# Performance work log

Hardware: AMD Instinct MI355X
Metric: run time of the kernel (lower is better)

## Reference

```python
import jax, jax.numpy as jnp
import numpy as np

SE, SD, B = 400, 50, 32
H, IN, A = 512, 512, 128
VF, V = 1024, 32000

def _p(k, shape):
    return jax.random.normal(k, shape, dtype=jnp.float32) * 0.02

def setup_inputs() -> dict:
    key = jax.random.key(0)
    ks = jax.random.split(key, 24)
    inp = {
        'output_enc': jax.random.normal(ks[0], (SE, B, 2 * H), dtype=jnp.float32),
        'input_dec': jax.random.normal(ks[1], (SD, B, IN), dtype=jnp.float32),
        'hidden_enc': jax.random.normal(ks[2], (4, B, H), dtype=jnp.float32),
        'cell_state_enc': jax.random.normal(ks[3], (4, B, H), dtype=jnp.float32),
        # LSTM layer 0 (PyTorch gate order i,f,g,o)
        'W_ih0': _p(ks[4], (4 * H, IN)), 'W_hh0': _p(ks[5], (4 * H, H)),
        'b_ih0': _p(ks[6], (4 * H,)), 'b_hh0': _p(ks[7], (4 * H,)),
        # LSTM layer 1
        'W_ih1': _p(ks[8], (4 * H, H)), 'W_hh1': _p(ks[9], (4 * H, H)),
        'b_ih1': _p(ks[10], (4 * H,)), 'b_hh1': _p(ks[11], (4 * H,)),
        # reduce_dim: 2H -> H
        'W_red': _p(ks[12], (H, 2 * H)), 'b_red': _p(ks[13], (H,)),
        # attention: 3H -> A, attn_out: A -> 1 (no bias)
        'W_att': _p(ks[14], (A, 3 * H)), 'b_att': _p(ks[15], (A,)),
        'v_att': _p(ks[16], (1, A)),
        # vocab MLP: 3H -> VF -> V
        'W_v1': _p(ks[17], (VF, 3 * H)), 'b_v1': _p(ks[18], (VF,)),
        'W_v2': _p(ks[19], (V, VF)), 'b_v2': _p(ks[20], (V,)),
    }
    return inp

def _forward(output_enc, input_dec, hidden_enc, cell_state_enc,
             W_ih0, W_hh0, b_ih0, b_hh0, W_ih1, W_hh1, b_ih1, b_hh1,
             W_red, b_red, W_att, b_att, v_att, W_v1, b_v1, W_v2, b_v2):
    # first_word=True path: fold bidirectional encoder state [4,B,H] -> [2,B,2H] -> [2,B,H]
    old_enc = jnp.concatenate([hidden_enc[0:2], hidden_enc[2:]], axis=-1)
    old_cell = jnp.concatenate([cell_state_enc[0:2], cell_state_enc[2:]], axis=-1)
    new_enc = old_enc @ W_red.T + b_red    # [2,B,H]
    new_cell = old_cell @ W_red.T + b_red  # [2,B,H]

    def lstm_cell(x, h, c, W_ih, W_hh, b_ih, b_hh):
        g = x @ W_ih.T + h @ W_hh.T + b_ih + b_hh
        i, f, gg, o = jnp.split(g, 4, axis=-1)
        c_new = jax.nn.sigmoid(f) * c + jax.nn.sigmoid(i) * jnp.tanh(gg)
        h_new = jax.nn.sigmoid(o) * jnp.tanh(c_new)
        return h_new, c_new

    def step(carry, x_t):
        h0, c0, h1, c1 = carry
        h0, c0 = lstm_cell(x_t, h0, c0, W_ih0, W_hh0, b_ih0, b_hh0)
        h1, c1 = lstm_cell(h0, h1, c1, W_ih1, W_hh1, b_ih1, b_hh1)
        return (h0, c0, h1, c1), h1

    init = (new_enc[0], new_cell[0], new_enc[1], new_cell[1])
    (h0f, c0f, h1f, c1f), output_dec = jax.lax.scan(step, init, input_dec)
    hidden_dec = jnp.stack([h0f, h1f])       # [2,B,H]
    cell_state_dec = jnp.stack([c0f, c1f])   # [2,B,H]

    # Additive (Bahdanau) attention, batched over all decoder timesteps.
    # cat order is (output_enc, output_dec) -> first 2H cols of W_att hit encoder.
    enc_part = output_enc @ W_att[:, :2 * H].T              # [Se,B,A]
    dec_part = output_dec @ W_att[:, 2 * H:].T + b_att       # [Sd,B,A]
    e = jnp.tanh(enc_part[:, None] + dec_part[None])         # [Se,Sd,B,A]
    e = jnp.einsum('stba,a->stb', e, v_att[0])               # [Se,Sd,B]
    attn = jax.nn.softmax(e, axis=0)                         # softmax over encoder dim
    context = jnp.einsum('stb,sbe->tbe', attn, output_enc)   # [Sd,B,2H]

    pv_in = jnp.concatenate([output_dec, context], axis=-1)  # [Sd,B,3H]
    pvocab = (pv_in @ W_v1.T + b_v1) @ W_v2.T + b_v2         # [Sd,B,V]
    return pvocab, (hidden_dec, cell_state_dec)

def reference(output_enc, input_dec, hidden_enc, cell_state_enc,
              W_ih0, W_hh0, b_ih0, b_hh0, W_ih1, W_hh1, b_ih1, b_hh1,
              W_red, b_red, W_att, b_att, v_att, W_v1, b_v1, W_v2, b_v2):
    return _forward(output_enc, input_dec, hidden_enc, cell_state_enc,
                    W_ih0, W_hh0, b_ih0, b_hh0, W_ih1, W_hh1, b_ih1, b_hh1,
                    W_red, b_red, W_att, b_att, v_att, W_v1, b_v1, W_v2, b_v2)
```

## Files before the change

### kernel.cpp

```cpp
#include <hip/hip_runtime.h>
#include <cstdint>

#define DEV __device__ __forceinline__

typedef short bfrag __attribute__((ext_vector_type(8)));
typedef float ffrag __attribute__((ext_vector_type(4)));

constexpr int SE = 400, SD = 50, BB = 32;
constexpr int HH = 512, INW = 512, AA = 128;
constexpr int VF = 1024, VV = 32000;
constexpr int G4 = 2048;

DEV ushort f2bf(float f) {
    uint32_t u = __float_as_uint(f);
    u = (u + 0x7FFF + ((u >> 16) & 1)) >> 16;
    return (ushort)u;
}
DEV float bf2f(ushort u) { return __uint_as_float(((uint32_t)u) << 16); }
DEV float sigm_(float x) { return 1.f / (1.f + __expf(-x)); }
DEV float tanh_(float x) { float e = __expf(2.f * x); return 1.f - 2.f / (e + 1.f); }
DEV int imin(int a, int b) { return a < b ? a : b; }
DEV int imax(int a, int b) { return a > b ? a : b; }

DEV void gload_lds16(const void* g, void* l) {
    __builtin_amdgcn_global_load_lds((const __attribute__((address_space(1))) uint32_t*)g,
                                     (__attribute__((address_space(3))) uint32_t*)l, 16, 0, 0);
}

__global__ __launch_bounds__(256) void k_cvt_flat(const float* __restrict__ s,
                                                  ushort* __restrict__ d, long n4) {
    long i = (long)blockIdx.x * 256 + threadIdx.x;
    if (i >= n4) return;
    float4 v = ((const float4*)s)[i];
    ushort4 o;
    o.x = f2bf(v.x); o.y = f2bf(v.y); o.z = f2bf(v.z); o.w = f2bf(v.w);
    ((ushort4*)d)[i] = o;
}

__global__ __launch_bounds__(256) void k_cvt_strided(const float* __restrict__ s,
                                                     ushort* __restrict__ d,
                                                     int rows, int cols, int sstride, int soff,
                                                     int dstride, int doff) {
    int i = blockIdx.x * 256 + threadIdx.x;
    int c4n = cols >> 2;
    if (i >= rows * c4n) return;
    int r = i / c4n, c = (i - r * c4n) * 4;
    float4 v = *(const float4*)(s + (size_t)r * sstride + soff + c);
    ushort4 o;
    o.x = f2bf(v.x); o.y = f2bf(v.y); o.z = f2bf(v.z); o.w = f2bf(v.w);
    *(ushort4*)(d + (size_t)r * dstride + doff + c) = o;
}

__global__ __launch_bounds__(256) void k_bsum(const float* __restrict__ bi0, const float* __restrict__ bh0,
                                              const float* __restrict__ bi1, const float* __restrict__ bh1,
                                              float* __restrict__ bsum0, float* __restrict__ bsum1) {
    int i = blockIdx.x * 256 + threadIdx.x;
    if (i >= G4) return;
    bsum0[i] = bi0[i] + bh0[i];
    bsum1[i] = bi1[i] + bh1[i];
}

__global__ __launch_bounds__(256) void k_fold(const float* __restrict__ hid,
                                              const float* __restrict__ cel,
                                              const float* __restrict__ W_red,
                                              const float* __restrict__ b_red,
                                              float* __restrict__ h0m,
                                              float* __restrict__ c0, float* __restrict__ c1,
                                              ushort* __restrict__ AB) {
    int tid = threadIdx.x;
    int j = blockIdx.x * 256 + tid;
    int b = blockIdx.y;
    int l = blockIdx.z & 1;
    bool is_c = blockIdx.z >> 1;
    const float* src = is_c ? cel : hid;
    __shared__ float xs[1024];
    for (int i = tid; i < 512; i += 256) {
        xs[i]       = src[((size_t)l * BB + b) * HH + i];
        xs[512 + i] = src[((size_t)(l + 2) * BB + b) * HH + i];
    }
    __syncthreads();
    const float4* w  = (const float4*)(W_red + (size_t)j * 1024);
    const float4* xv = (const float4*)xs;
    float acc = b_red[j];
    for (int k = 0; k < 256; k++) {
        float4 a = w[k], x = xv[k];
        acc += a.x * x.x + a.y * x.y + a.z * x.z + a.w * x.w;
    }
    if (is_c) {
        (l ? c1 : c0)[(size_t)b * HH + j] = acc;
    } else {
        if (l == 0) {
            h0m[(size_t)b * HH + j] = acc;
            AB[(size_t)32 * 1024 + (size_t)b * 1024 + j] = f2bf(acc);
        } else {
            AB[(size_t)b * 1024 + 512 + j] = f2bf(acc);
        }
    }
}

__global__ __launch_bounds__(256) void k_cell(const ushort* __restrict__ Aprev,
                                              const ushort* __restrict__ W0,
                                              const ushort* __restrict__ W1,
                                              const float* __restrict__ gx,
                                              const float* __restrict__ bsum1,
                                              float* __restrict__ c0, float* __restrict__ c1,
                                              float* __restrict__ h0m,
                                              float* __restrict__ od1,
                                              ushort* __restrict__ od1_bf,
                                              ushort* __restrict__ ABdst,
                                              int do_l0, int do_l1) {
    const int layer = blockIdx.y;
    if (layer == 0 && !do_l0) return;
    if (layer == 1 && !do_l1) return;
    const int jb = blockIdx.x;
    const int tid = threadIdx.x, wave = tid >> 6, lane = tid & 63;
    const int lr = lane & 15, lk = lane >> 4;
    const int K = layer ? 1024 : 512;
    const ushort* Wm = layer ? W1 : W0;
    const int wstride = layer ? 1024 : 512;
    const int n0 = wave * 512 + jb * 16;

    const ushort* arow0 = Aprev + (size_t)lr * 1024;
    const ushort* arow1 = Aprev + (size_t)(16 + lr) * 1024;
    const ushort* wrow  = Wm + (size_t)(n0 + lr) * wstride;

    ffrag acc0 = {0.f, 0.f, 0.f, 0.f}, acc1 = {0.f, 0.f, 0.f, 0.f};
    #pragma unroll 4
    for (int k0 = 0; k0 < K; k0 += 32) {
        bfrag a0 = *(const bfrag*)(arow0 + k0 + lk * 8);
        bfrag a1 = *(const bfrag*)(arow1 + k0 + lk * 8);
        bfrag bw = *(const bfrag*)(wrow + k0 + lk * 8);
        acc0 = __builtin_amdgcn_mfma_f32_16x16x32_bf16(a0, bw, acc0, 0, 0, 0);
        acc1 = __builtin_amdgcn_mfma_f32_16x16x32_bf16(a1, bw, acc1, 0, 0, 0);
    }

    __shared__ float gl[4][32][16];
    #pragma unroll
    for (int r = 0; r < 4; r++) {
        gl[wave][lk * 4 + r][lr]      = acc0[r];
        gl[wave][16 + lk * 4 + r][lr] = acc1[r];
    }
    __syncthreads();

    for (int e = tid; e < 512; e += 256) {
        int b = e >> 4, jj = e & 15;
        int j = jb * 16 + jj;
        float gi = gl[0][b][jj], gf = gl[1][b][jj], gg = gl[2][b][jj], go = gl[3][b][jj];
        if (layer == 0) {
            const float* gxp = gx + (size_t)b * G4;
            gi += gxp[j]; gf += gxp[512 + j]; gg += gxp[1024 + j]; go += gxp[1536 + j];
        } else {
            gi += bsum1[j]; gf += bsum1[512 + j]; gg += bsum1[1024 + j]; go += bsum1[1536 + j];
        }
        float* cc = layer ? c1 : c0;
        size_t ci = (size_t)b * HH + j;
        float cn = sigm_(gf) * cc[ci] + sigm_(gi) * tanh_(gg);
        cc[ci] = cn;
        float hn = sigm_(go) * tanh_(cn);
        ushort hb = f2bf(hn);
        if (layer == 0) {
            h0m[ci] = hn;
            ABdst[(size_t)b * 1024 + j] = hb;
        } else {
            od1[ci] = hn;
            od1_bf[ci] = hb;
            ABdst[(size_t)b * 1024 + 512 + j] = hb;
        }
    }
}

__global__ __launch_bounds__(256) void k_states(const float* __restrict__ h0,
                                                const float* __restrict__ h1,
                                                const float* __restrict__ c0,
                                                const float* __restrict__ c1,
                                                float* __restrict__ out) {
    int i = blockIdx.x * 256 + threadIdx.x;
    if (i >= BB * HH) return;
    out[i]               = h0[i];
    out[BB * HH + i]     = h1[i];
    out[2 * BB * HH + i] = c0[i];
    out[3 * BB * HH + i] = c1[i];
}

template <int OUT_BF16>
__global__ __launch_bounds__(256) void k_gemm128(const ushort* __restrict__ X,
                                                 const ushort* __restrict__ W,
                                                 float* __restrict__ Cf,
                                                 ushort* __restrict__ Cb,
                                                 const float* __restrict__ bias,
                                                 int M, int N, int K, int nmt) {
    __shared__ ushort As[128 * 32];
    __shared__ ushort Bs[128 * 32];
    const int tid = threadIdx.x;
    const int wave = tid >> 6, lane = tid & 63;
    const int lr = lane & 15, lk = lane >> 4;
    const int wm = wave >> 1, wn = wave & 1;

    int nwg = gridDim.x, flat = blockIdx.x;
    int q = nwg >> 3, r = nwg & 7;
    int xcd = flat & 7, idx = flat >> 3;
    int wg = (xcd < r ? xcd * (q + 1) : r * (q + 1) + (xcd - r) * q) + idx;
    const int m0 = (wg % nmt) * 128, n0 = (wg / nmt) * 128;

    ffrag acc[4][4];
    #pragma unroll
    for (int i = 0; i < 4; i++)
        #pragma unroll
        for (int j = 0; j < 4; j++) acc[i][j] = (ffrag){0.f, 0.f, 0.f, 0.f};

    const int srow = wave * 16 + (lane >> 2);
    const int scol = (lane & 3) * 8;
    const int ar0 = imin(m0 + srow, M - 1);
    const int ar1 = imin(m0 + 64 + srow, M - 1);
    const ushort* Agp0 = X + (size_t)ar0 * K + scol;
    const ushort* Agp1 = X + (size_t)ar1 * K + scol;
    const ushort* Bgp0 = W + (size_t)(n0 + srow) * K + scol;
    const ushort* Bgp1 = W + (size_t)(n0 + 64 + srow) * K + scol;
    ushort* AsW0 = As + wave * 512;
    ushort* AsW1 = As + 2048 + wave * 512;
    ushort* BsW0 = Bs + wave * 512;
    ushort* BsW1 = Bs + 2048 + wave * 512;

    for (int k0 = 0; k0 < K; k0 += 32) {
        gload_lds16(Agp0 + k0, AsW0);
        gload_lds16(Agp1 + k0, AsW1);
        gload_lds16(Bgp0 + k0, BsW0);
        gload_lds16(Bgp1 + k0, BsW1);
        __syncthreads();
        bfrag a[4], bfr[4];
        #pragma unroll
        for (int mf = 0; mf < 4; mf++)
            a[mf] = *(const bfrag*)&As[(wm * 64 + mf * 16 + lr) * 32 + lk * 8];
        #pragma unroll
        for (int nf = 0; nf < 4; nf++)
            bfr[nf] = *(const bfrag*)&Bs[(wn * 64 + nf * 16 + lr) * 32 + lk * 8];
        #pragma unroll
        for (int mf = 0; mf < 4; mf++)
            #pragma unroll
            for (int nf = 0; nf < 4; nf++)
                acc[mf][nf] = __builtin_amdgcn_mfma_f32_16x16x32_bf16(a[mf], bfr[nf], acc[mf][nf], 0, 0, 0);
        __syncthreads();
    }

    #pragma unroll
    for (int mf = 0; mf < 4; mf++) {
        int rbase = m0 + wm * 64 + mf * 16 + lk * 4;
        #pragma unroll
        for (int nf = 0; nf < 4; nf++) {
            int cc = n0 + wn * 64 + nf * 16 + lr;
            float bv = bias ? bias[cc] : 0.f;
            #pragma unroll
            for (int rr = 0; rr < 4; rr++) {
                int row = rbase + rr;
                if (row < M) {
                    float v = acc[mf][nf][rr] + bv;
                    if (OUT_BF16) Cb[(size_t)row * N + cc] = f2bf(v);
                    else          Cf[(size_t)row * N + cc] = v;
                }
            }
        }
    }
}

__global__ __launch_bounds__(256) void k_scores(const float* __restrict__ encp,
                                                const float* __restrict__ decp,
                                                const float* __restrict__ v_att,
                                                float* __restrict__ attn) {
    int t = blockIdx.x, b = blockIdx.y, tid = threadIdx.x;
    __shared__ float dp[128], vv[128];
    __shared__ float e_lds[400];
    __shared__ float red[8];
    if (tid < 128) {
        dp[tid] = decp[((size_t)t * BB + b) * AA + tid];
        vv[tid] = v_att[tid];
    }
    __syncthreads();
    for (int s = tid; s < SE; s += 256) {
        const float* ep = encp + ((size_t)s * BB + b) * AA;
        float a0 = 0.f;
        #pragma unroll 4
        for (int a = 0; a < AA; a++) a0 += vv[a] * tanh_(ep[a] + dp[a]);
        e_lds[s] = a0;
    }
    __syncthreads();
    float m = -1e30f;
    for (int s = tid; s < SE; s += 256) m = fmaxf(m, e_lds[s]);
    #pragma unroll
    for (int o = 32; o > 0; o >>= 1) m = fmaxf(m, __shfl_xor(m, o));
    if ((tid & 63) == 0) red[tid >> 6] = m;
    __syncthreads();
    m = fmaxf(fmaxf(red[0], red[1]), fmaxf(red[2], red[3]));
    float sum = 0.f;
    for (int s = tid; s < SE; s += 256) {
        float ex = __expf(e_lds[s] - m);
        e_lds[s] = ex;
        sum += ex;
    }
    #pragma unroll
    for (int o = 32; o > 0; o >>= 1) sum += __shfl_xor(sum, o);
    if ((tid & 63) == 0) red[4 + (tid >> 6)] = sum;
    __syncthreads();
    float inv = 1.f / (red[4] + red[5] + red[6] + red[7]);
    for (int s = tid; s < SE; s += 256)
        attn[((size_t)b * SD + t) * SE + s] = e_lds[s] * inv;
}

__global__ __launch_bounds__(256) void k_context(const float* __restrict__ attn,
                                                 const ushort* __restrict__ oe_bf,
                                                 float* __restrict__ ctx) {
    int b = blockIdx.x, nc = blockIdx.y, th = blockIdx.z, tid = threadIdx.x;
    __shared__ float at[25][400];
    const float* ap = attn + ((size_t)b * SD + th * 25) * SE;
    for (int i = tid; i < 25 * 400; i += 256) at[i / 400][i % 400] = ap[i];
    __syncthreads();
    int n = nc * 256 + tid;
    float acc[25];
    #pragma unroll
    for (int i = 0; i < 25; i++) acc[i] = 0.f;
    for (int s = 0; s < SE; s++) {
        float v = bf2f(oe_bf[((size_t)s * BB + b) * 1024 + n]);
        #pragma unroll
        for (int tt = 0; tt < 25; tt++) acc[tt] += at[tt][s] * v;
    }
    #pragma unroll
    for (int tt = 0; tt < 25; tt++)
        ctx[(((size_t)(th * 25 + tt)) * BB + b) * 1024 + n] = acc[tt];
}

__global__ __launch_bounds__(256) void k_concat(const ushort* __restrict__ od_bf,
                                                const float* __restrict__ ctx,
                                                ushort* __restrict__ x1) {
    int i = blockIdx.x * 256 + threadIdx.x;
    if (i >= 1600 * 384) return;
    int rr = i / 384, c4 = (i - rr * 384) * 4;
    ushort4 o;
    if (c4 < 512) {
        o = *(const ushort4*)(od_bf + (size_t)rr * 512 + c4);
    } else {
        float4 v = *(const float4*)(ctx + (size_t)rr * 1024 + (c4 - 512));
        o.x = f2bf(v.x); o.y = f2bf(v.y); o.z = f2bf(v.z); o.w = f2bf(v.w);
    }
    *(ushort4*)(x1 + (size_t)rr * 1536 + c4) = o;
}

extern "C" void kernel_launch(void* const* d_in, const int* in_sizes, int n_in,
                              void* d_out, int out_size, void* d_ws, size_t ws_size,
                              hipStream_t stream) {
    const float* output_enc = (const float*)d_in[0];
    const float* input_dec  = (const float*)d_in[1];
    const float* hidden_enc = (const float*)d_in[2];
    const float* cell_enc   = (const float*)d_in[3];
    const float* W_ih0 = (const float*)d_in[4],  *W_hh0 = (const float*)d_in[5];
    const float* b_ih0 = (const float*)d_in[6],  *b_hh0 = (const float*)d_in[7];
    const float* W_ih1 = (const float*)d_in[8],  *W_hh1 = (const float*)d_in[9];
    const float* b_ih1 = (const float*)d_in[10], *b_hh1 = (const float*)d_in[11];
    const float* W_red = (const float*)d_in[12], *b_red = (const float*)d_in[13];
    const float* W_att = (const float*)d_in[14], *b_att = (const float*)d_in[15];
    const float* v_att = (const float*)d_in[16];
    const float* W_v1  = (const float*)d_in[17], *b_v1 = (const float*)d_in[18];
    const float* W_v2  = (const float*)d_in[19], *b_v2 = (const float*)d_in[20];

    char* ws = (char*)d_ws;
    size_t off = 0;
    auto alloc = [&](size_t bytes) -> void* {
        void* p = ws + off;
        off += (bytes + 255) & ~(size_t)255;
        return p;
    };
    float*  h0m    = (float*)alloc(BB * HH * 4);
    float*  c0     = (float*)alloc(BB * HH * 4);
    float*  c1     = (float*)alloc(BB * HH * 4);
    ushort* AB     = (ushort*)alloc(2 * BB * 1024 * 2);
    float*  od     = (float*)alloc((size_t)SD * BB * HH * 4);
    ushort* od_bf  = (ushort*)alloc((size_t)SD * BB * HH * 2);
    ushort* xd_bf  = (ushort*)alloc((size_t)SD * BB * INW * 2);
    ushort* wih0b  = (ushort*)alloc((size_t)G4 * 512 * 2);
    ushort* whh0b  = (ushort*)alloc((size_t)G4 * 512 * 2);
    ushort* w1cat  = (ushort*)alloc((size_t)G4 * 1024 * 2);
    float*  bsum0  = (float*)alloc(G4 * 4);
    float*  bsum1  = (float*)alloc(G4 * 4);
    float*  gx0    = (float*)alloc((size_t)SD * BB * G4 * 4);
    ushort* oe_bf  = (ushort*)alloc((size_t)SE * BB * 1024 * 2);
    ushort* wae    = (ushort*)alloc((size_t)AA * 1024 * 2);
    ushort* wad    = (ushort*)alloc((size_t)AA * 512 * 2);
    float*  encp   = (float*)alloc((size_t)SE * BB * AA * 4);
    float*  decp   = (float*)alloc((size_t)SD * BB * AA * 4);
    float*  attn   = (float*)alloc((size_t)BB * SD * SE * 4);
    float*  ctx    = (float*)alloc((size_t)SD * BB * 1024 * 4);
    ushort* x1     = (ushort*)alloc((size_t)1600 * 1536 * 2);
    ushort* wv1    = (ushort*)alloc((size_t)VF * 1536 * 2);
    ushort* y1     = (ushort*)alloc((size_t)1600 * VF * 2);
    ushort* wv2    = (ushort*)alloc((size_t)VV * 1024 * 2);

    k_cvt_flat<<<800, 256, 0, stream>>>(input_dec, xd_bf, (long)SD * BB * INW / 4);
    k_cvt_flat<<<12800, 256, 0, stream>>>(output_enc, oe_bf, (long)SE * BB * 1024 / 4);
    k_cvt_flat<<<1024, 256, 0, stream>>>(W_ih0, wih0b, (long)G4 * 512 / 4);
    k_cvt_flat<<<1024, 256, 0, stream>>>(W_hh0, whh0b, (long)G4 * 512 / 4);
    k_cvt_strided<<<1024, 256, 0, stream>>>(W_ih1, w1cat, G4, 512, 512, 0, 1024, 0);
    k_cvt_strided<<<1024, 256, 0, stream>>>(W_hh1, w1cat, G4, 512, 512, 0, 1024, 512);
    k_cvt_strided<<<128, 256, 0, stream>>>(W_att, wae, AA, 1024, 1536, 0, 1024, 0);
    k_cvt_strided<<<64, 256, 0, stream>>>(W_att, wad, AA, 512, 1536, 1024, 512, 0);
    k_cvt_flat<<<1536, 256, 0, stream>>>(W_v1, wv1, (long)VF * 1536 / 4);
    k_cvt_flat<<<32000, 256, 0, stream>>>(W_v2, wv2, (long)VV * 1024 / 4);
    k_bsum<<<8, 256, 0, stream>>>(b_ih0, b_hh0, b_ih1, b_hh1, bsum0, bsum1);

    k_fold<<<dim3(2, 32, 4), 256, 0, stream>>>(hidden_enc, cell_enc, W_red, b_red,
                                               h0m, c0, c1, AB);

    k_gemm128<0><<<13 * 16, 256, 0, stream>>>(xd_bf, wih0b, gx0, nullptr, bsum0,
                                              SD * BB, G4, 512, 13);

    for (int i = 0; i <= SD; i++) {
        const ushort* Aprev = AB + (size_t)((i + 1) & 1) * BB * 1024;
        ushort* ABdst = AB + (size_t)(i & 1) * BB * 1024;
        int t1c = (i > 0) ? (i - 1) : 0;
        k_cell<<<dim3(32, 2), 256, 0, stream>>>(Aprev, whh0b, w1cat,
                                                gx0 + (size_t)i * BB * G4, bsum1,
                                                c0, c1, h0m,
                                                od + (size_t)t1c * BB * HH,
                                                od_bf + (size_t)t1c * BB * HH,
                                                ABdst, (int)(i < SD), (int)(i > 0));
    }
    k_states<<<64, 256, 0, stream>>>(h0m, od + (size_t)(SD - 1) * BB * HH, c0, c1,
                                     (float*)d_out + (size_t)SD * BB * VV);

    k_gemm128<0><<<100, 256, 0, stream>>>(oe_bf, wae, encp, nullptr,
                                          (const float*)nullptr, SE * BB, AA, 1024, 100);
    k_gemm128<0><<<13, 256, 0, stream>>>(od_bf, wad, decp, nullptr,
                                         b_att, SD * BB, AA, 512, 13);
    k_scores<<<dim3(SD, BB), 256, 0, stream>>>(encp, decp, v_att, attn);
    k_context<<<dim3(32, 4, 2), 256, 0, stream>>>(attn, oe_bf, ctx);

    k_concat<<<2400, 256, 0, stream>>>(od_bf, ctx, x1);
    k_gemm128<1><<<13 * 8, 256, 0, stream>>>(x1, wv1, nullptr, y1, b_v1,
                                             1600, VF, 1536, 13);
    k_gemm128<0><<<13 * 250, 256, 0, stream>>>(y1, wv2, (float*)d_out, nullptr, b_v2,
                                               1600, VV, 1024, 13);
    (void)in_sizes; (void)n_in; (void)out_size; (void)ws_size;
}
```

Before: 1.669 ms.

## Batch conversions, double-buffer GEMM, fuse concat into producers, vectorize scores

The ten conversion launches are merged into two multi-segment kernels that find their segment from a per-launch table. The bf16 GEMM now double-buffers its LDS tiles, so the next K-tile loads while the current one is computed. The LSTM cell and context kernels write bf16 directly into the concatenated vocab-MLP input, which removes the fp32 context buffer and the separate concat kernel. The scores loop reads float4 vectors and the context loop is unrolled by four. The cost is double the GEMM shared memory, which may lower occupancy.

```diff
diff --git a/kernel.cpp b/kernel.cpp
--- a/kernel.cpp
+++ b/kernel.cpp
@@ -20,35 +20,47 @@
 DEV float sigm_(float x) { return 1.f / (1.f + __expf(-x)); }
 DEV float tanh_(float x) { float e = __expf(2.f * x); return 1.f - 2.f / (e + 1.f); }
 DEV int imin(int a, int b) { return a < b ? a : b; }
-DEV int imax(int a, int b) { return a > b ? a : b; }
 
 DEV void gload_lds16(const void* g, void* l) {
     __builtin_amdgcn_global_load_lds((const __attribute__((address_space(1))) uint32_t*)g,
                                      (__attribute__((address_space(3))) uint32_t*)l, 16, 0, 0);
 }
 
-__global__ __launch_bounds__(256) void k_cvt_flat(const float* __restrict__ s,
-                                                  ushort* __restrict__ d, long n4) {
-    long i = (long)blockIdx.x * 256 + threadIdx.x;
-    if (i >= n4) return;
-    float4 v = ((const float4*)s)[i];
+struct CvtFlatTab {
+    const float* src[6];
+    ushort* dst[6];
+    int blk_end[6];
+    int nseg;
+};
+__global__ __launch_bounds__(256) void k_cvt_multi(CvtFlatTab t) {
+    int blk = blockIdx.x, seg = 0;
+    while (seg < t.nseg - 1 && blk >= t.blk_end[seg]) seg++;
+    int base = seg ? t.blk_end[seg - 1] : 0;
+    long i = (long)(blk - base) * 256 + threadIdx.x;
+    float4 v = ((const float4*)t.src[seg])[i];
     ushort4 o;
     o.x = f2bf(v.x); o.y = f2bf(v.y); o.z = f2bf(v.z); o.w = f2bf(v.w);
-    ((ushort4*)d)[i] = o;
-}
-
-__global__ __launch_bounds__(256) void k_cvt_strided(const float* __restrict__ s,
-                                                     ushort* __restrict__ d,
-                                                     int rows, int cols, int sstride, int soff,
-                                                     int dstride, int doff) {
-    int i = blockIdx.x * 256 + threadIdx.x;
-    int c4n = cols >> 2;
-    if (i >= rows * c4n) return;
+    ((ushort4*)t.dst[seg])[i] = o;
+}
+
+struct CvtStrTab {
+    const float* src[4];
+    ushort* dst[4];
+    int ss[4], so[4], ds[4], dofs[4], c4n[4];
+    int blk_end[4];
+    int nseg;
+};
+__global__ __launch_bounds__(256) void k_cvt_str_multi(CvtStrTab t) {
+    int blk = blockIdx.x, seg = 0;
+    while (seg < t.nseg - 1 && blk >= t.blk_end[seg]) seg++;
+    int base = seg ? t.blk_end[seg - 1] : 0;
+    int i = (blk - base) * 256 + threadIdx.x;
+    int c4n = t.c4n[seg];
     int r = i / c4n, c = (i - r * c4n) * 4;
-    float4 v = *(const float4*)(s + (size_t)r * sstride + soff + c);
+    float4 v = *(const float4*)(t.src[seg] + (size_t)r * t.ss[seg] + t.so[seg] + c);
     ushort4 o;
     o.x = f2bf(v.x); o.y = f2bf(v.y); o.z = f2bf(v.z); o.w = f2bf(v.w);
-    *(ushort4*)(d + (size_t)r * dstride + doff + c) = o;
+    *(ushort4*)(t.dst[seg] + (size_t)r * t.ds[seg] + t.dofs[seg] + c) = o;
 }
 
 __global__ __launch_bounds__(256) void k_bsum(const float* __restrict__ bi0, const float* __restrict__ bh0,
@@ -107,6 +119,7 @@
                                               float* __restrict__ h0m,
                                               float* __restrict__ od1,
                                               ushort* __restrict__ od1_bf,
+                                              ushort* __restrict__ x1row,
                                               ushort* __restrict__ ABdst,
                                               int do_l0, int do_l1) {
     const int layer = blockIdx.y;
@@ -164,6 +177,7 @@
         } else {
             od1[ci] = hn;
             od1_bf[ci] = hb;
+            x1row[(size_t)b * 1536 + j] = hb;
             ABdst[(size_t)b * 1024 + 512 + j] = hb;
         }
     }
@@ -189,8 +203,8 @@
                                                  ushort* __restrict__ Cb,
                                                  const float* __restrict__ bias,
                                                  int M, int N, int K, int nmt) {
-    __shared__ ushort As[128 * 32];
-    __shared__ ushort Bs[128 * 32];
+    __shared__ ushort As[2][4096];
+    __shared__ ushort Bs[2][4096];
     const int tid = threadIdx.x;
     const int wave = tid >> 6, lane = tid & 63;
     const int lr = lane & 15, lk = lane >> 4;
@@ -216,31 +230,41 @@
     const ushort* Agp1 = X + (size_t)ar1 * K + scol;
     const ushort* Bgp0 = W + (size_t)(n0 + srow) * K + scol;
     const ushort* Bgp1 = W + (size_t)(n0 + 64 + srow) * K + scol;
-    ushort* AsW0 = As + wave * 512;
-    ushort* AsW1 = As + 2048 + wave * 512;
-    ushort* BsW0 = Bs + wave * 512;
-    ushort* BsW1 = Bs + 2048 + wave * 512;
-
-    for (int k0 = 0; k0 < K; k0 += 32) {
-        gload_lds16(Agp0 + k0, AsW0);
-        gload_lds16(Agp1 + k0, AsW1);
-        gload_lds16(Bgp0 + k0, BsW0);
-        gload_lds16(Bgp1 + k0, BsW1);
-        __syncthreads();
+
+    auto stage = [&](int buf, int k0) {
+        ushort* AsW = As[buf] + wave * 512;
+        ushort* BsW = Bs[buf] + wave * 512;
+        gload_lds16(Agp0 + k0, AsW);
+        gload_lds16(Agp1 + k0, AsW + 2048);
+        gload_lds16(Bgp0 + k0, BsW);
+        gload_lds16(Bgp1 + k0, BsW + 2048);
+    };
+    auto compute = [&](int buf) {
         bfrag a[4], bfr[4];
         #pragma unroll
         for (int mf = 0; mf < 4; mf++)
-            a[mf] = *(const bfrag*)&As[(wm * 64 + mf * 16 + lr) * 32 + lk * 8];
+            a[mf] = *(const bfrag*)&As[buf][(wm * 64 + mf * 16 + lr) * 32 + lk * 8];
         #pragma unroll
         for (int nf = 0; nf < 4; nf++)
-            bfr[nf] = *(const bfrag*)&Bs[(wn * 64 + nf * 16 + lr) * 32 + lk * 8];
+            bfr[nf] = *(const bfrag*)&Bs[buf][(wn * 64 + nf * 16 + lr) * 32 + lk * 8];
         #pragma unroll
         for (int mf = 0; mf < 4; mf++)
             #pragma unroll
             for (int nf = 0; nf < 4; nf++)
                 acc[mf][nf] = __builtin_amdgcn_mfma_f32_16x16x32_bf16(a[mf], bfr[nf], acc[mf][nf], 0, 0, 0);
+    };
+
+    const int nt = K >> 5;
+    stage(0, 0);
+    __syncthreads();
+    int cur = 0;
+    for (int t = 0; t < nt - 1; ++t) {
+        stage(cur ^ 1, (t + 1) << 5);
+        compute(cur);
         __syncthreads();
-    }
+        cur ^= 1;
+    }
+    compute(cur);
 
     #pragma unroll
     for (int mf = 0; mf < 4; mf++) {
@@ -275,11 +299,17 @@
         vv[tid] = v_att[tid];
     }
     __syncthreads();
+    const float4* dp4 = (const float4*)dp;
+    const float4* vv4 = (const float4*)vv;
     for (int s = tid; s < SE; s += 256) {
-        const float* ep = encp + ((size_t)s * BB + b) * AA;
+        const float4* ep4 = (const float4*)(encp + ((size_t)s * BB + b) * AA);
         float a0 = 0.f;
         #pragma unroll 4
-        for (int a = 0; a < AA; a++) a0 += vv[a] * tanh_(ep[a] + dp[a]);
+        for (int a = 0; a < AA / 4; a++) {
+            float4 e = ep4[a], d = dp4[a], v = vv4[a];
+            a0 += v.x * tanh_(e.x + d.x) + v.y * tanh_(e.y + d.y)
+                + v.z * tanh_(e.z + d.z) + v.w * tanh_(e.w + d.w);
+        }
         e_lds[s] = a0;
     }
     __syncthreads();
@@ -307,7 +337,7 @@
 
 __global__ __launch_bounds__(256) void k_context(const float* __restrict__ attn,
                                                  const ushort* __restrict__ oe_bf,
-                                                 float* __restrict__ ctx) {
+                                                 ushort* __restrict__ x1) {
     int b = blockIdx.x, nc = blockIdx.y, th = blockIdx.z, tid = threadIdx.x;
     __shared__ float at[25][400];
     const float* ap = attn + ((size_t)b * SD + th * 25) * SE;
@@ -317,30 +347,21 @@
     float acc[25];
     #pragma unroll
     for (int i = 0; i < 25; i++) acc[i] = 0.f;
-    for (int s = 0; s < SE; s++) {
-        float v = bf2f(oe_bf[((size_t)s * BB + b) * 1024 + n]);
-        #pragma unroll
-        for (int tt = 0; tt < 25; tt++) acc[tt] += at[tt][s] * v;
-    }
-    #pragma unroll
-    for (int tt = 0; tt < 25; tt++)
-        ctx[(((size_t)(th * 25 + tt)) * BB + b) * 1024 + n] = acc[tt];
-}
-
-__global__ __launch_bounds__(256) void k_concat(const ushort* __restrict__ od_bf,
-                                                const float* __restrict__ ctx,
-                                                ushort* __restrict__ x1) {
-    int i = blockIdx.x * 256 + threadIdx.x;
-    if (i >= 1600 * 384) return;
-    int rr = i / 384, c4 = (i - rr * 384) * 4;
-    ushort4 o;
-    if (c4 < 512) {
-        o = *(const ushort4*)(od_bf + (size_t)rr * 512 + c4);
-    } else {
-        float4 v = *(const float4*)(ctx + (size_t)rr * 1024 + (c4 - 512));
-        o.x = f2bf(v.x); o.y = f2bf(v.y); o.z = f2bf(v.z); o.w = f2bf(v.w);
-    }
-    *(ushort4*)(x1 + (size_t)rr * 1536 + c4) = o;
+    for (int s = 0; s < SE; s += 4) {
+        float v0 = bf2f(oe_bf[((size_t)(s + 0) * BB + b) * 1024 + n]);
+        float v1 = bf2f(oe_bf[((size_t)(s + 1) * BB + b) * 1024 + n]);
+        float v2 = bf2f(oe_bf[((size_t)(s + 2) * BB + b) * 1024 + n]);
+        float v3 = bf2f(oe_bf[((size_t)(s + 3) * BB + b) * 1024 + n]);
+        #pragma unroll
+        for (int tt = 0; tt < 25; tt++)
+            acc[tt] += at[tt][s] * v0 + at[tt][s + 1] * v1
+                     + at[tt][s + 2] * v2 + at[tt][s + 3] * v3;
+    }
+    #pragma unroll
+    for (int tt = 0; tt < 25; tt++) {
+        int row = (th * 25 + tt) * BB + b;
+        x1[(size_t)row * 1536 + 512 + n] = f2bf(acc[tt]);
+    }
 }
 
 extern "C" void kernel_launch(void* const* d_in, const int* in_sizes, int n_in,
@@ -386,22 +407,41 @@
     float*  encp   = (float*)alloc((size_t)SE * BB * AA * 4);
     float*  decp   = (float*)alloc((size_t)SD * BB * AA * 4);
     float*  attn   = (float*)alloc((size_t)BB * SD * SE * 4);
-    float*  ctx    = (float*)alloc((size_t)SD * BB * 1024 * 4);
     ushort* x1     = (ushort*)alloc((size_t)1600 * 1536 * 2);
     ushort* wv1    = (ushort*)alloc((size_t)VF * 1536 * 2);
     ushort* y1     = (ushort*)alloc((size_t)1600 * VF * 2);
     ushort* wv2    = (ushort*)alloc((size_t)VV * 1024 * 2);
 
-    k_cvt_flat<<<800, 256, 0, stream>>>(input_dec, xd_bf, (long)SD * BB * INW / 4);
-    k_cvt_flat<<<12800, 256, 0, stream>>>(output_enc, oe_bf, (long)SE * BB * 1024 / 4);
-    k_cvt_flat<<<1024, 256, 0, stream>>>(W_ih0, wih0b, (long)G4 * 512 / 4);
-    k_cvt_flat<<<1024, 256, 0, stream>>>(W_hh0, whh0b, (long)G4 * 512 / 4);
-    k_cvt_strided<<<1024, 256, 0, stream>>>(W_ih1, w1cat, G4, 512, 512, 0, 1024, 0);
-    k_cvt_strided<<<1024, 256, 0, stream>>>(W_hh1, w1cat, G4, 512, 512, 0, 1024, 512);
-    k_cvt_strided<<<128, 256, 0, stream>>>(W_att, wae, AA, 1024, 1536, 0, 1024, 0);
-    k_cvt_strided<<<64, 256, 0, stream>>>(W_att, wad, AA, 512, 1536, 1024, 512, 0);
-    k_cvt_flat<<<1536, 256, 0, stream>>>(W_v1, wv1, (long)VF * 1536 / 4);
-    k_cvt_flat<<<32000, 256, 0, stream>>>(W_v2, wv2, (long)VV * 1024 / 4);
+    {
+        CvtFlatTab t;
+        int nb = 0, k = 0;
+        auto add = [&](const float* s, ushort* d, long n) {
+            t.src[k] = s; t.dst[k] = d; nb += (int)(n / 1024); t.blk_end[k] = nb; k++;
+        };
+        add(input_dec, xd_bf, (long)SD * BB * INW);
+        add(output_enc, oe_bf, (long)SE * BB * 1024);
+        add(W_ih0, wih0b, (long)G4 * 512);
+        add(W_hh0, whh0b, (long)G4 * 512);
+        add(W_v1, wv1, (long)VF * 1536);
+        add(W_v2, wv2, (long)VV * 1024);
+        t.nseg = k;
+        k_cvt_multi<<<nb, 256, 0, stream>>>(t);
+    }
+    {
+        CvtStrTab t;
+        int nb = 0, k = 0;
+        auto add = [&](const float* s, ushort* d, int rows, int cols, int ss, int so, int ds, int dofs) {
+            t.src[k] = s; t.dst[k] = d; t.ss[k] = ss; t.so[k] = so;
+            t.ds[k] = ds; t.dofs[k] = dofs; t.c4n[k] = cols / 4;
+            nb += rows * cols / 1024; t.blk_end[k] = nb; k++;
+        };
+        add(W_ih1, w1cat, G4, 512, 512, 0, 1024, 0);
+        add(W_hh1, w1cat, G4, 512, 512, 0, 1024, 512);
+        add(W_att, wae, AA, 1024, 1536, 0, 1024, 0);
+        add(W_att, wad, AA, 512, 1536, 1024, 512, 0);
+        t.nseg = k;
+        k_cvt_str_multi<<<nb, 256, 0, stream>>>(t);
+    }
     k_bsum<<<8, 256, 0, stream>>>(b_ih0, b_hh0, b_ih1, b_hh1, bsum0, bsum1);
 
     k_fold<<<dim3(2, 32, 4), 256, 0, stream>>>(hidden_enc, cell_enc, W_red, b_red,
@@ -419,6 +459,7 @@
                                                 c0, c1, h0m,
                                                 od + (size_t)t1c * BB * HH,
                                                 od_bf + (size_t)t1c * BB * HH,
+                                                x1 + (size_t)t1c * BB * 1536,
                                                 ABdst, (int)(i < SD), (int)(i > 0));
     }
     k_states<<<64, 256, 0, stream>>>(h0m, od + (size_t)(SD - 1) * BB * HH, c0, c1,
@@ -429,9 +470,8 @@
     k_gemm128<0><<<13, 256, 0, stream>>>(od_bf, wad, decp, nullptr,
                                          b_att, SD * BB, AA, 512, 13);
     k_scores<<<dim3(SD, BB), 256, 0, stream>>>(encp, decp, v_att, attn);
-    k_context<<<dim3(32, 4, 2), 256, 0, stream>>>(attn, oe_bf, ctx);
-
-    k_concat<<<2400, 256, 0, stream>>>(od_bf, ctx, x1);
+    k_context<<<dim3(32, 4, 2), 256, 0, stream>>>(attn, oe_bf, x1);
+
     k_gemm128<1><<<13 * 8, 256, 0, stream>>>(x1, wv1, nullptr, y1, b_v1,
                                              1600, VF, 1536, 13);
     k_gemm128<0><<<13 * 250, 256, 0, stream>>>(y1, wv2, (float*)d_out, nullptr, b_v2,
```

Result: faster. 1.631 ms (-2.3%).
